# Kernel optimization log

Hardware: AMD Instinct MI355X
Metric: run time of the kernel (lower is better)

The kernel has to match this reference:

```python
import jax, jax.numpy as jnp
import numpy as np

# lower-triangular <-> 3x3 symmetric matrix index maps (match torch_lotri2mat/mat2lotri)
LOTRI = np.array([[0, 1, 3], [1, 2, 4], [3, 4, 5]])
ROWS = np.array([0, 1, 1, 2, 2, 2])
COLS = np.array([0, 0, 1, 0, 1, 2])
NUM_NEWTON_ITERS = 6


def det3(A):
    # A: (N,3,3)
    return (A[:, 0, 0] * (A[:, 1, 1] * A[:, 2, 2] - A[:, 1, 2] * A[:, 2, 1])
            - A[:, 0, 1] * (A[:, 1, 0] * A[:, 2, 2] - A[:, 1, 2] * A[:, 2, 0])
            + A[:, 0, 2] * (A[:, 1, 0] * A[:, 2, 1] - A[:, 1, 1] * A[:, 2, 0]))


def inv3(A):
    # closed-form 3x3 inverse via adjugate; A: (N,3,3)
    c00 = A[:, 1, 1] * A[:, 2, 2] - A[:, 1, 2] * A[:, 2, 1]
    c01 = A[:, 0, 2] * A[:, 2, 1] - A[:, 0, 1] * A[:, 2, 2]
    c02 = A[:, 0, 1] * A[:, 1, 2] - A[:, 0, 2] * A[:, 1, 1]
    c10 = A[:, 1, 2] * A[:, 2, 0] - A[:, 1, 0] * A[:, 2, 2]
    c11 = A[:, 0, 0] * A[:, 2, 2] - A[:, 0, 2] * A[:, 2, 0]
    c12 = A[:, 0, 2] * A[:, 1, 0] - A[:, 0, 0] * A[:, 1, 2]
    c20 = A[:, 1, 0] * A[:, 2, 1] - A[:, 1, 1] * A[:, 2, 0]
    c21 = A[:, 0, 1] * A[:, 2, 0] - A[:, 0, 0] * A[:, 2, 1]
    c22 = A[:, 0, 0] * A[:, 1, 1] - A[:, 0, 1] * A[:, 1, 0]
    adj = jnp.stack([jnp.stack([c00, c01, c02], -1),
                     jnp.stack([c10, c11, c12], -1),
                     jnp.stack([c20, c21, c22], -1)], -2)  # (N,3,3)
    det = (A[:, 0, 0] * c00 + A[:, 0, 1] * c10 + A[:, 0, 2] * c20)
    return adj / det[:, None, None]


def trilinear_warp(img, ddf):
    # img: (B,C,H,W,D), ddf: (B,3,H,W,D) in voxel units; border padding (clamped corners)
    B, C, H, W, D = img.shape
    base = jnp.stack(jnp.meshgrid(jnp.arange(H), jnp.arange(W), jnp.arange(D),
                                  indexing='ij'), 0).astype(img.dtype)  # (3,H,W,D)
    coords = base[None] + ddf                                           # (B,3,H,W,D)
    c0 = jnp.floor(coords)
    frac = coords - c0
    c0i = c0.astype(jnp.int32)
    dims = jnp.array([H, W, D], jnp.int32).reshape(1, 3, 1, 1, 1)
    lo = jnp.clip(c0i, 0, dims - 1)
    hi = jnp.clip(c0i + 1, 0, dims - 1)
    imgf = img.reshape(B, C, H * W * D)

    def gather(xi, yi, zi):
        lin = (xi * W + yi) * D + zi                      # (B,H,W,D)
        idx = jnp.broadcast_to(lin.reshape(B, 1, -1), (B, C, H * W * D))
        return jnp.take_along_axis(imgf, idx, axis=2).reshape(B, C, H, W, D)

    fx, fy, fz = frac[:, 0, None], frac[:, 1, None], frac[:, 2, None]  # (B,1,H,W,D)
    x0, y0, z0 = lo[:, 0], lo[:, 1], lo[:, 2]
    x1, y1, z1 = hi[:, 0], hi[:, 1], hi[:, 2]
    out = jnp.zeros_like(img)
    for xi, wx in ((x0, 1.0 - fx), (x1, fx)):
        for yi, wy in ((y0, 1.0 - fy), (y1, fy)):
            for zi, wz in ((z0, 1.0 - fz), (z1, fz)):
                out = out + wx * wy * wz * gather(xi, yi, zi)
    return out


def ddf_jacobian(ddf):
    # Jacobian of the deformation phi(x)=x+ddf(x): J = I + d(ddf_i)/dx_j (central differences)
    rows = []
    for i in range(3):
        g = jnp.gradient(ddf[:, i], axis=(1, 2, 3))  # list of 3 arrays (B,H,W,D)
        rows.append(jnp.stack(g, axis=1))
    J = jnp.stack(rows, axis=1)                      # (B,3,3,H,W,D)
    eye = jnp.eye(3, dtype=ddf.dtype).reshape(1, 3, 3, 1, 1, 1)
    return J + eye


def newton_polar_det(X, n_iters):
    # Newton iteration for polar decomposition with determinant scaling
    U = X
    for _ in range(n_iters):
        zeta = jnp.abs(det3(U)) ** (-1.0 / 3.0)
        zU = zeta[:, None, None] * U
        U = 0.5 * (zU + inv3(jnp.swapaxes(zU, -1, -2)))
    return U


def setup_inputs() -> dict:
    key = jax.random.key(0)
    k1, k2 = jax.random.split(key)
    B, H, W, D = 2, 128, 128, 128
    dti = jax.random.normal(k1, (B, 6, H, W, D), dtype=jnp.float32)
    # smooth, realistic displacement field so J = I + grad(ddf) is well-conditioned
    g = jnp.stack(jnp.meshgrid(jnp.arange(H), jnp.arange(W), jnp.arange(D),
                               indexing='ij'), 0).astype(jnp.float32) / H  # (3,H,W,D)
    two_pi = 2.0 * jnp.pi
    amp = 2.0
    ddf = amp * jnp.stack([jnp.sin(two_pi * (g[0] + 0.5 * g[1])),
                           jnp.cos(two_pi * (g[1] + 0.5 * g[2])),
                           jnp.sin(two_pi * (g[2] + 0.5 * g[0]))], 0)  # (3,H,W,D)
    ddf = jnp.broadcast_to(ddf[None], (B, 3, H, W, D))
    ddf = ddf + 0.02 * jax.random.normal(k2, (B, 3, H, W, D), dtype=jnp.float32)
    return {"dti": dti, "ddf": ddf}


def reference(dti, ddf):
    B, _, H, W, D = dti.shape
    # 1) warp the lower-triangular DTI with trilinear interpolation (border padding)
    warped_lotri = trilinear_warp(dti, ddf)              # (B,6,H,W,D)
    # 2) lotri -> 3x3 symmetric matrices, absorb spatial dims
    Dmat = warped_lotri[:, LOTRI]                        # (B,3,3,H,W,D)
    Dns = Dmat.transpose(0, 3, 4, 5, 1, 2).reshape(-1, 3, 3)
    # 3) Jacobian of DDF, absorb spatial dims
    J = ddf_jacobian(ddf)                                # (B,3,3,H,W,D)
    Jns = J.transpose(0, 3, 4, 5, 1, 2).reshape(-1, 3, 3)
    # 4) rotation from polar decomposition (Newton, det scaling)
    R = newton_polar_det(Jns, NUM_NEWTON_ITERS)          # (N,3,3)
    # 5) finite-strain reorientation: R^T D R per voxel
    out_ns = jnp.einsum('nji,njk,nkl->nil', R, Dns, R)
    # 6) expand spatial dims, mat -> lotri
    out_mat = out_ns.reshape(B, H, W, D, 3, 3).transpose(0, 4, 5, 1, 2, 3)
    return out_mat[:, ROWS, COLS]                        # (B,6,H,W,D)
```

## Files before the change

kernel.cpp:

```cpp
#include <hip/hip_runtime.h>

#define NH 128
#define NW 128
#define ND 128
#define HWD (NH * NW * ND)
#define NWD (NW * ND)
#define NB 2

typedef float f32x2 __attribute__((ext_vector_type(2)));

__global__ __launch_bounds__(256) void warp_dti_kernel(
    const float* __restrict__ dti,
    const float* __restrict__ ddf,
    float* __restrict__ out)
{
    const int blk   = blockIdx.x;
    const int b     = blk >> 13;
    const int blkin = blk & 8191;
    const int tid   = threadIdx.x;
    const int sp    = (blkin << 8) | tid;
    const int d     = tid & (ND - 1);
    const int w     = ((blkin & 63) << 1) | (tid >> 7);
    const int h     = blkin >> 6;

    const int dbase = b * 3 * HWD;

    const int oh_m = (h > 0)      ? -NWD : 0;
    const int oh_p = (h < NH - 1) ?  NWD : 0;
    const int ow_m = (w > 0)      ? -ND  : 0;
    const int ow_p = (w < NW - 1) ?  ND  : 0;
    const int od_m = (d > 0)      ? -1   : 0;
    const int od_p = (d < ND - 1) ?  1   : 0;

    float uc[3], hm[3], hp[3], wm[3], wp[3], dm[3], dp[3];
#pragma unroll
    for (int c = 0; c < 3; ++c) {
        const float* p = ddf + dbase + c * HWD;
        uc[c] = p[sp];
        hm[c] = p[sp + oh_m];  hp[c] = p[sp + oh_p];
        wm[c] = p[sp + ow_m];  wp[c] = p[sp + ow_p];
        dm[c] = p[sp + od_m];  dp[c] = p[sp + od_p];
    }

    const float sh = (oh_m == 0 || oh_p == 0) ? 1.0f : 0.5f;
    const float sw = (ow_m == 0 || ow_p == 0) ? 1.0f : 0.5f;
    const float sd = (od_m == 0 || od_p == 0) ? 1.0f : 0.5f;

    float U[3][3];
#pragma unroll
    for (int c = 0; c < 3; ++c) {
        U[c][0] = sh * (hp[c] - hm[c]);
        U[c][1] = sw * (wp[c] - wm[c]);
        U[c][2] = sd * (dp[c] - dm[c]);
    }
    U[0][0] += 1.0f; U[1][1] += 1.0f; U[2][2] += 1.0f;

    const float cx = (float)h + uc[0];
    const float cy = (float)w + uc[1];
    const float cz = (float)d + uc[2];
    const float flx = floorf(cx), fly = floorf(cy), flz = floorf(cz);
    const float fx = cx - flx, fy = cy - fly, fz = cz - flz;
    const int x0 = (int)flx, y0 = (int)fly, z0 = (int)flz;
    const int xa = min(max(x0,     0), NH - 1), xb = min(max(x0 + 1, 0), NH - 1);
    const int ya = min(max(y0,     0), NW - 1), yb = min(max(y0 + 1, 0), NW - 1);
    const int pa = min(max(z0, 0), ND - 2);

    unsigned voffs[4];
    voffs[0] = (unsigned)(((xa * NW + ya) * ND) + pa) * 4u;
    voffs[1] = (unsigned)(((xa * NW + yb) * ND) + pa) * 4u;
    voffs[2] = (unsigned)(((xb * NW + ya) * ND) + pa) * 4u;
    voffs[3] = (unsigned)(((xb * NW + yb) * ND) + pa) * 4u;

    const float* bases[6];
#pragma unroll
    for (int ch = 0; ch < 6; ++ch)
        bases[ch] = dti + (size_t)(b * 6 + ch) * HWD;

    __builtin_amdgcn_sched_barrier(0);
    f32x2 g[6][4];
#pragma unroll
    for (int ch = 0; ch < 6; ++ch)
#pragma unroll
        for (int c = 0; c < 4; ++c)
            asm volatile("global_load_dwordx2 %0, %1, %2"
                         : "=v"(g[ch][c])
                         : "v"(voffs[c]), "s"(bases[ch]));

#pragma unroll
    for (int it = 0; it < 6; ++it) {
        float c00 = U[1][1]*U[2][2] - U[1][2]*U[2][1];
        float c01 = U[0][2]*U[2][1] - U[0][1]*U[2][2];
        float c02 = U[0][1]*U[1][2] - U[0][2]*U[1][1];
        float c10 = U[1][2]*U[2][0] - U[1][0]*U[2][2];
        float c11 = U[0][0]*U[2][2] - U[0][2]*U[2][0];
        float c12 = U[0][2]*U[1][0] - U[0][0]*U[1][2];
        float c20 = U[1][0]*U[2][1] - U[1][1]*U[2][0];
        float c21 = U[0][1]*U[2][0] - U[0][0]*U[2][1];
        float c22 = U[0][0]*U[1][1] - U[0][1]*U[1][0];
        float det = U[0][0]*c00 + U[0][1]*c10 + U[0][2]*c20;

        float l    = __log2f(fabsf(det));
        float zeta = __builtin_amdgcn_exp2f(-0.33333333333333333f * l);
        float s    = copysignf(zeta * zeta, det);
        float hz = 0.5f * zeta;
        float hs = 0.5f * s;

        float n00 = hz*U[0][0] + c00*hs;
        float n01 = hz*U[0][1] + c10*hs;
        float n02 = hz*U[0][2] + c20*hs;
        float n10 = hz*U[1][0] + c01*hs;
        float n11 = hz*U[1][1] + c11*hs;
        float n12 = hz*U[1][2] + c21*hs;
        float n20 = hz*U[2][0] + c02*hs;
        float n21 = hz*U[2][1] + c12*hs;
        float n22 = hz*U[2][2] + c22*hs;
        U[0][0]=n00; U[0][1]=n01; U[0][2]=n02;
        U[1][0]=n10; U[1][1]=n11; U[1][2]=n12;
        U[2][0]=n20; U[2][1]=n21; U[2][2]=n22;
    }

    const float wza = 1.0f - fz, wzb = fz;
    const float wv0 = ((z0 <= ND - 2) ? wza : 0.0f) + ((z0 <= -1) ? wzb : 0.0f);
    const float wv1 = ((z0 >= ND - 1) ? wza : 0.0f) + ((z0 >=  0) ? wzb : 0.0f);
    const float wxa = 1.0f - fx, wya = 1.0f - fy;
    float wxy[4];
    wxy[0] = wxa * wya;  wxy[1] = wxa * fy;
    wxy[2] = fx  * wya;  wxy[3] = fx  * fy;
    float wA[4], wB[4];
#pragma unroll
    for (int c = 0; c < 4; ++c) { wA[c] = wxy[c] * wv0; wB[c] = wxy[c] * wv1; }

    asm volatile("s_waitcnt vmcnt(0)" ::: "memory");
    __builtin_amdgcn_sched_barrier(0);

    float acc[6] = {0.f, 0.f, 0.f, 0.f, 0.f, 0.f};
#pragma unroll
    for (int c = 0; c < 4; ++c)
#pragma unroll
        for (int ch = 0; ch < 6; ++ch)
            acc[ch] = fmaf(wA[c], g[ch][c].x, fmaf(wB[c], g[ch][c].y, acc[ch]));

    float Dm[3][3];
    Dm[0][0] = acc[0]; Dm[0][1] = acc[1]; Dm[0][2] = acc[3];
    Dm[1][0] = acc[1]; Dm[1][1] = acc[2]; Dm[1][2] = acc[4];
    Dm[2][0] = acc[3]; Dm[2][1] = acc[4]; Dm[2][2] = acc[5];

    float M[3][3];
#pragma unroll
    for (int i = 0; i < 3; ++i)
#pragma unroll
        for (int k = 0; k < 3; ++k)
            M[i][k] = U[0][i]*Dm[0][k] + U[1][i]*Dm[1][k] + U[2][i]*Dm[2][k];

    float T00 = M[0][0]*U[0][0] + M[0][1]*U[1][0] + M[0][2]*U[2][0];
    float T10 = M[1][0]*U[0][0] + M[1][1]*U[1][0] + M[1][2]*U[2][0];
    float T11 = M[1][0]*U[0][1] + M[1][1]*U[1][1] + M[1][2]*U[2][1];
    float T20 = M[2][0]*U[0][0] + M[2][1]*U[1][0] + M[2][2]*U[2][0];
    float T21 = M[2][0]*U[0][1] + M[2][1]*U[1][1] + M[2][2]*U[2][1];
    float T22 = M[2][0]*U[0][2] + M[2][1]*U[1][2] + M[2][2]*U[2][2];

    const int obase = b * 6 * HWD;
    out[obase + 0 * HWD + sp] = T00;
    out[obase + 1 * HWD + sp] = T10;
    out[obase + 2 * HWD + sp] = T11;
    out[obase + 3 * HWD + sp] = T20;
    out[obase + 4 * HWD + sp] = T21;
    out[obase + 5 * HWD + sp] = T22;
}

extern "C" void kernel_launch(void* const* d_in, const int* in_sizes, int n_in,
                              void* d_out, int out_size, void* d_ws, size_t ws_size,
                              hipStream_t stream) {
    const float* dti = (const float*)d_in[0];
    const float* ddf = (const float*)d_in[1];
    float* o = (float*)d_out;
    const int n = NB * HWD;
    warp_dti_kernel<<<n / 256, 256, 0, stream>>>(dti, ddf, o);
}
```

Baseline: 265.5 us.

## Split DTI gathers into two phases interleaved with halves of Newton iterations

Issues the 24 trilinear gathers as two batches of 12 (three channels each). Each batch overlaps three of the six Newton polar iterations before the wait. This halves the number of live gather registers, aiming for higher occupancy while keeping some latency hiding. The cost is a second full memory wait per thread and less in-flight memory parallelism per wave.

```diff
diff --git a/kernel.cpp b/kernel.cpp
--- a/kernel.cpp
+++ b/kernel.cpp
@@ -8,6 +8,43 @@
 #define NB 2
 
 typedef float f32x2 __attribute__((ext_vector_type(2)));
+
+#define SB() __builtin_amdgcn_sched_barrier(0)
+
+__device__ __forceinline__ void newton3(float U[3][3]) {
+#pragma unroll
+    for (int it = 0; it < 3; ++it) {
+        float c00 = U[1][1]*U[2][2] - U[1][2]*U[2][1];
+        float c01 = U[0][2]*U[2][1] - U[0][1]*U[2][2];
+        float c02 = U[0][1]*U[1][2] - U[0][2]*U[1][1];
+        float c10 = U[1][2]*U[2][0] - U[1][0]*U[2][2];
+        float c11 = U[0][0]*U[2][2] - U[0][2]*U[2][0];
+        float c12 = U[0][2]*U[1][0] - U[0][0]*U[1][2];
+        float c20 = U[1][0]*U[2][1] - U[1][1]*U[2][0];
+        float c21 = U[0][1]*U[2][0] - U[0][0]*U[2][1];
+        float c22 = U[0][0]*U[1][1] - U[0][1]*U[1][0];
+        float det = U[0][0]*c00 + U[0][1]*c10 + U[0][2]*c20;
+
+        float l    = __log2f(fabsf(det));
+        float zeta = __builtin_amdgcn_exp2f(-0.33333333333333333f * l);
+        float s    = copysignf(zeta * zeta, det);
+        float hz = 0.5f * zeta;
+        float hs = 0.5f * s;
+
+        float n00 = hz*U[0][0] + c00*hs;
+        float n01 = hz*U[0][1] + c10*hs;
+        float n02 = hz*U[0][2] + c20*hs;
+        float n10 = hz*U[1][0] + c01*hs;
+        float n11 = hz*U[1][1] + c11*hs;
+        float n12 = hz*U[1][2] + c21*hs;
+        float n20 = hz*U[2][0] + c02*hs;
+        float n21 = hz*U[2][1] + c12*hs;
+        float n22 = hz*U[2][2] + c22*hs;
+        U[0][0]=n00; U[0][1]=n01; U[0][2]=n02;
+        U[1][0]=n10; U[1][1]=n11; U[1][2]=n12;
+        U[2][0]=n20; U[2][1]=n21; U[2][2]=n22;
+    }
+}
 
 __global__ __launch_bounds__(256) void warp_dti_kernel(
     const float* __restrict__ dti,
@@ -71,54 +108,6 @@
     voffs[2] = (unsigned)(((xb * NW + ya) * ND) + pa) * 4u;
     voffs[3] = (unsigned)(((xb * NW + yb) * ND) + pa) * 4u;
 
-    const float* bases[6];
-#pragma unroll
-    for (int ch = 0; ch < 6; ++ch)
-        bases[ch] = dti + (size_t)(b * 6 + ch) * HWD;
-
-    __builtin_amdgcn_sched_barrier(0);
-    f32x2 g[6][4];
-#pragma unroll
-    for (int ch = 0; ch < 6; ++ch)
-#pragma unroll
-        for (int c = 0; c < 4; ++c)
-            asm volatile("global_load_dwordx2 %0, %1, %2"
-                         : "=v"(g[ch][c])
-                         : "v"(voffs[c]), "s"(bases[ch]));
-
-#pragma unroll
-    for (int it = 0; it < 6; ++it) {
-        float c00 = U[1][1]*U[2][2] - U[1][2]*U[2][1];
-        float c01 = U[0][2]*U[2][1] - U[0][1]*U[2][2];
-        float c02 = U[0][1]*U[1][2] - U[0][2]*U[1][1];
-        float c10 = U[1][2]*U[2][0] - U[1][0]*U[2][2];
-        float c11 = U[0][0]*U[2][2] - U[0][2]*U[2][0];
-        float c12 = U[0][2]*U[1][0] - U[0][0]*U[1][2];
-        float c20 = U[1][0]*U[2][1] - U[1][1]*U[2][0];
-        float c21 = U[0][1]*U[2][0] - U[0][0]*U[2][1];
-        float c22 = U[0][0]*U[1][1] - U[0][1]*U[1][0];
-        float det = U[0][0]*c00 + U[0][1]*c10 + U[0][2]*c20;
-
-        float l    = __log2f(fabsf(det));
-        float zeta = __builtin_amdgcn_exp2f(-0.33333333333333333f * l);
-        float s    = copysignf(zeta * zeta, det);
-        float hz = 0.5f * zeta;
-        float hs = 0.5f * s;
-
-        float n00 = hz*U[0][0] + c00*hs;
-        float n01 = hz*U[0][1] + c10*hs;
-        float n02 = hz*U[0][2] + c20*hs;
-        float n10 = hz*U[1][0] + c01*hs;
-        float n11 = hz*U[1][1] + c11*hs;
-        float n12 = hz*U[1][2] + c21*hs;
-        float n20 = hz*U[2][0] + c02*hs;
-        float n21 = hz*U[2][1] + c12*hs;
-        float n22 = hz*U[2][2] + c22*hs;
-        U[0][0]=n00; U[0][1]=n01; U[0][2]=n02;
-        U[1][0]=n10; U[1][1]=n11; U[1][2]=n12;
-        U[2][0]=n20; U[2][1]=n21; U[2][2]=n22;
-    }
-
     const float wza = 1.0f - fz, wzb = fz;
     const float wv0 = ((z0 <= ND - 2) ? wza : 0.0f) + ((z0 <= -1) ? wzb : 0.0f);
     const float wv1 = ((z0 >= ND - 1) ? wza : 0.0f) + ((z0 >=  0) ? wzb : 0.0f);
@@ -130,15 +119,72 @@
 #pragma unroll
     for (int c = 0; c < 4; ++c) { wA[c] = wxy[c] * wv0; wB[c] = wxy[c] * wv1; }
 
+    const float* bases[6];
+#pragma unroll
+    for (int ch = 0; ch < 6; ++ch)
+        bases[ch] = dti + (size_t)(b * 6 + ch) * HWD;
+
+    float acc[6];
+
+    SB();
+    f32x2 g0[3][4];
+#pragma unroll
+    for (int ch = 0; ch < 3; ++ch)
+#pragma unroll
+        for (int c = 0; c < 4; ++c)
+            asm volatile("global_load_dwordx2 %0, %1, %2"
+                         : "=v"(g0[ch][c])
+                         : "v"(voffs[c]), "s"(bases[ch]));
+    SB();
+
+    newton3(U);
+
     asm volatile("s_waitcnt vmcnt(0)" ::: "memory");
-    __builtin_amdgcn_sched_barrier(0);
-
-    float acc[6] = {0.f, 0.f, 0.f, 0.f, 0.f, 0.f};
-#pragma unroll
-    for (int c = 0; c < 4; ++c)
-#pragma unroll
-        for (int ch = 0; ch < 6; ++ch)
-            acc[ch] = fmaf(wA[c], g[ch][c].x, fmaf(wB[c], g[ch][c].y, acc[ch]));
+    SB();
+#pragma unroll
+    for (int ch = 0; ch < 3; ++ch)
+#pragma unroll
+        for (int c = 0; c < 4; ++c)
+            asm volatile("" : "+v"(g0[ch][c]));
+
+#pragma unroll
+    for (int ch = 0; ch < 3; ++ch) {
+        float a = 0.0f;
+#pragma unroll
+        for (int c = 0; c < 4; ++c)
+            a = fmaf(wA[c], g0[ch][c].x, fmaf(wB[c], g0[ch][c].y, a));
+        acc[ch] = a;
+    }
+    SB();
+
+    f32x2 g1[3][4];
+#pragma unroll
+    for (int ch = 0; ch < 3; ++ch)
+#pragma unroll
+        for (int c = 0; c < 4; ++c)
+            asm volatile("global_load_dwordx2 %0, %1, %2"
+                         : "=v"(g1[ch][c])
+                         : "v"(voffs[c]), "s"(bases[ch + 3]));
+    SB();
+
+    newton3(U);
+
+    asm volatile("s_waitcnt vmcnt(0)" ::: "memory");
+    SB();
+#pragma unroll
+    for (int ch = 0; ch < 3; ++ch)
+#pragma unroll
+        for (int c = 0; c < 4; ++c)
+            asm volatile("" : "+v"(g1[ch][c]));
+
+#pragma unroll
+    for (int ch = 0; ch < 3; ++ch) {
+        float a = 0.0f;
+#pragma unroll
+        for (int c = 0; c < 4; ++c)
+            a = fmaf(wA[c], g1[ch][c].x, fmaf(wB[c], g1[ch][c].y, a));
+        acc[ch + 3] = a;
+    }
 
     float Dm[3][3];
     Dm[0][0] = acc[0]; Dm[0][1] = acc[1]; Dm[0][2] = acc[3];
```

New measurement: 271.1 us. +2.1%, slower.
